# Optimization experiments

Hardware: AMD Instinct MI355X
Metric: run time of the kernel (lower is better)

Reference implementation:

```python
import jax, jax.numpy as jnp
import numpy as np

N = 100000
E = 3200000
CH_IN = 128
HID = 128
CH_OUT = 3


def setup_inputs() -> dict:
    key = jax.random.key(0)
    ks = jax.random.split(key, 16)
    def lin(kw, fan_in, fan_out):
        bound = 1.0 / np.sqrt(fan_in)
        kw1, kw2 = jax.random.split(kw)
        W = jax.random.uniform(kw1, (fan_in, fan_out), jnp.float32, -bound, bound)
        b = jax.random.uniform(kw2, (fan_out,), jnp.float32, -bound, bound)
        return W, b
    x = jax.random.normal(ks[0], (N, CH_IN), jnp.float32)
    edge_index = jax.random.randint(ks[1], (2, E), 0, N, jnp.int64)
    W1, b1 = lin(ks[2], CH_IN, HID)
    W2, b2 = lin(ks[3], HID, HID)
    lw1, lb1 = lin(ks[4], HID, HID)
    lw2, lb2 = lin(ks[5], HID, HID)
    lw3, lb3 = lin(ks[6], HID, HID)
    lw4, lb4 = lin(ks[7], HID, CH_OUT)
    return {"x": x, "edge_index": edge_index,
            "W1": W1, "b1": b1, "W2": W2, "b2": b2,
            "lw1": lw1, "lb1": lb1, "lw2": lw2, "lb2": lb2,
            "lw3": lw3, "lb3": lb3, "lw4": lw4, "lb4": lb4}


def gcn_conv(x, W, b, src, dst, n_nodes):
    xw = x @ W  # [N, H]
    ew = jnp.ones(src.shape[0], x.dtype)
    deg = jax.ops.segment_sum(ew, dst, num_segments=n_nodes) + 2.0  # +2 from improved self-loop
    dinv = jnp.where(deg > 0, jax.lax.rsqrt(deg), 0.0)
    norm = dinv[src] * dinv[dst]  # [E]
    agg = jax.ops.segment_sum(xw[src] * norm[:, None], dst, num_segments=n_nodes)
    # self-loop contribution: weight 2 * dinv[i]^2 * xw[i]
    agg = agg + xw * (2.0 * dinv * dinv)[:, None]
    return agg + b


def reference(x, edge_index, W1, b1, W2, b2, lw1, lb1, lw2, lb2, lw3, lb3, lw4, lb4):
    src, dst = edge_index[0], edge_index[1]
    n = x.shape[0]
    h = jnp.tanh(gcn_conv(x, W1, b1, src, dst, n))
    h = jnp.tanh(gcn_conv(h, W2, b2, src, dst, n))
    # dropout in eval mode = identity
    h = jnp.tanh(h @ lw1 + lb1)
    h = jnp.tanh(h @ lw2 + lb2)
    h = jnp.tanh(h @ lw3 + lb3)
    return h @ lw4 + lb4
```

## Files before the change

kernel.cpp:

```cpp
#include <hip/hip_runtime.h>

typedef __attribute__((ext_vector_type(8))) short short8;
typedef __attribute__((ext_vector_type(4))) float floatx4;
typedef __attribute__((ext_vector_type(4))) unsigned int uintx4;
typedef unsigned int uint32;

__device__ inline float b2f(unsigned short u) {
    union { uint32 i; float f; } x; x.i = ((uint32)u) << 16; return x.f;
}
__device__ inline float bl(uint32 v) {
    union { uint32 i; float f; } x; x.i = v << 16; return x.f;
}
__device__ inline float bh(uint32 v) {
    union { uint32 i; float f; } x; x.i = v & 0xffff0000u; return x.f;
}
__device__ inline unsigned short f2b(float f) {
    union { float f; uint32 u; } x; x.f = f;
    uint32 r = x.u + 0x7fffu + ((x.u >> 16) & 1u);
    return (unsigned short)(r >> 16);
}
__device__ inline float fast_tanh(float x) {
    float ax = __builtin_fabsf(x);
    float t = __builtin_amdgcn_exp2f(-2.8853900817779268f * ax);
    float r = (1.0f - t) * __builtin_amdgcn_rcpf(1.0f + t);
    return __builtin_copysignf(r, x);
}


#define CHUNK 8192
#define MAXBK 512
#define CAP   8704

__global__ __launch_bounds__(512, 2) void scatterb_k(const int* __restrict__ eidx,
                                                     uint32* __restrict__ bkt_cur,
                                                     uint32* __restrict__ packed, int E) {
    __shared__ uint32 hist[MAXBK];
    __shared__ uint32 hsc[MAXBK];
    __shared__ uint32 gbase[MAXBK];
    __shared__ uint32 lcur[MAXBK];
    __shared__ uint32 wsum[8];
    __shared__ uint32 stage[CHUNK];
    __shared__ unsigned short stgb[CHUNK];
    int t = threadIdx.x;
    int cbase = blockIdx.x * CHUNK;
    int n = E - cbase; if (n > CHUNK) n = CHUNK;

    hist[t] = 0;
    __syncthreads();
    int dreg[CHUNK / 512];
    int nt = 0;
    for (int i = t; i < n; i += 512) {
        int d = eidx[E + cbase + i];
        dreg[nt++] = d;
        atomicAdd(&hist[d >> 8], 1u);
    }
    __syncthreads();
    uint32 v = hist[t];
    uint32 x = v;
    int lane = t & 63;
#pragma unroll
    for (int off = 1; off < 64; off <<= 1) {
        uint32 y = __shfl_up(x, off);
        if (lane >= off) x += y;
    }
    if (lane == 63) wsum[t >> 6] = x;
    __syncthreads();
    uint32 pre = 0;
#pragma unroll
    for (int w = 0; w < 8; ++w) pre += (w < (t >> 6)) ? wsum[w] : 0;
    uint32 excl = x + pre - v;
    hsc[t] = excl;
    lcur[t] = excl;
    if (v) gbase[t] = (uint32)t * CAP + atomicAdd(&bkt_cur[t], v);
    __syncthreads();
    nt = 0;
    for (int i = t; i < n; i += 512) {
        int s = eidx[cbase + i];
        int d = dreg[nt++];
        int b = d >> 8;
        uint32 pos = atomicAdd(&lcur[b], 1u);
        stage[pos] = ((uint32)s << 8) | (uint32)(d & 255);
        stgb[pos] = (unsigned short)b;
    }
    __syncthreads();
    for (int i = t; i < n; i += 512) {
        int b = stgb[i];
        packed[gbase[b] + (i - hsc[b])] = stage[i];
    }
}


__global__ __launch_bounds__(256) void buildb_k(const uint32* __restrict__ packed,
                                                const uint32* __restrict__ bkt_cur,
                                                int* __restrict__ rowp,
                                                int* __restrict__ rowe,
                                                float* __restrict__ dinv,
                                                int* __restrict__ csr, int N,
                                                const float* __restrict__ w0,
                                                const float* __restrict__ w1,
                                                const float* __restrict__ w2,
                                                const float* __restrict__ w3,
                                                const float* __restrict__ w4,
                                                unsigned short* __restrict__ Wt_hi,
                                                unsigned short* __restrict__ Wt_lo) {
    __shared__ uint32 cnt[256];
    __shared__ uint32 cur[256];
    __shared__ uint32 wsum4[4];
    int t = threadIdx.x;
    int b = blockIdx.x;

    if (b < 40) {
        int widx = b >> 3;
        int f8 = ((b & 7) << 8) | t;
        const float* W;
        switch (widx) {
            case 0: W = w0; break;
            case 1: W = w1; break;
            case 2: W = w2; break;
            case 3: W = w3; break;
            default: W = w4; break;
        }
        int ct = f8 >> 8, kc = (f8 >> 6) & 3, quad = (f8 >> 4) & 3, r = f8 & 15;
        int c = ct * 16 + r;
        int kbase = kc * 32 + quad * 8;
        short8 hi8, lo8;
#pragma unroll
        for (int j = 0; j < 8; ++j) {
            float w = W[(kbase + j) * 128 + c];
            unsigned short h = f2b(w);
            hi8[j] = (short)h;
            lo8[j] = (short)f2b(w - b2f(h));
        }
        *(short8*)(Wt_hi + widx * 16384 + f8 * 8) = hi8;
        *(short8*)(Wt_lo + widx * 16384 + f8 * 8) = lo8;
    }

    uint32 base = (uint32)b * CAP;
    uint32 size = bkt_cur[b];
    int node0 = b << 8;

    cnt[t] = 0;
    __syncthreads();
    for (uint32 i = t; i < size; i += 256)
        atomicAdd(&cnt[packed[base + i] & 255u], 1u);
    __syncthreads();
    uint32 v = cnt[t];
    uint32 x = v;
    int lane = t & 63;
#pragma unroll
    for (int off = 1; off < 64; off <<= 1) {
        uint32 y = __shfl_up(x, off);
        if (lane >= off) x += y;
    }
    if (lane == 63) wsum4[t >> 6] = x;
    __syncthreads();
    uint32 pre = 0;
#pragma unroll
    for (int w = 0; w < 4; ++w) pre += (w < (t >> 6)) ? wsum4[w] : 0;
    uint32 loc = x + pre - v;
    cur[t] = loc;
    int node = node0 + t;
    if (node < N) {
        dinv[node] = rsqrtf((float)v + 2.0f);
        rowp[node] = (int)(base + loc);
        rowe[node] = (int)(base + loc + v);
    }
    __syncthreads();
    for (uint32 i = t; i < size; i += 256) {
        uint32 p = packed[base + i];
        uint32 pos = atomicAdd(&cur[p & 255u], 1u);
        csr[base + pos] = (int)(p >> 8);
    }
}


template <int ASRC>
__global__ __launch_bounds__(256, 4) void gemm_z_k(
    const void* __restrict__ Asrc,
    const unsigned short* __restrict__ Wt_hi,
    const unsigned short* __restrict__ Wt_lo,
    const float* __restrict__ dinv,
    unsigned short* __restrict__ out, int N) {
    int tid = threadIdx.x;
    if (blockIdx.x == 0 && tid < 64) {
        ((uint32*)out)[(size_t)N * 64 + tid] = 0;
    }
    int wave = tid >> 6, lane = tid & 63;
    int quad = lane >> 4, r = lane & 15;
    int m32 = blockIdx.x * 128 + wave * 32;

    short8 af[2][4];
#pragma unroll
    for (int s = 0; s < 2; ++s) {
        int rowA = m32 + s * 16 + r;
        if (rowA >= N) rowA = N - 1;
        if (ASRC == 0) {
            const float4* Af = (const float4*)Asrc;
#pragma unroll
            for (int kc = 0; kc < 4; ++kc) {
                float4 p0 = Af[((size_t)rowA * 128 + kc * 32 + quad * 8) >> 2];
                float4 p1 = Af[(((size_t)rowA * 128 + kc * 32 + quad * 8) >> 2) + 1];
                short8 a;
                a[0] = (short)f2b(p0.x); a[1] = (short)f2b(p0.y);
                a[2] = (short)f2b(p0.z); a[3] = (short)f2b(p0.w);
                a[4] = (short)f2b(p1.x); a[5] = (short)f2b(p1.y);
                a[6] = (short)f2b(p1.z); a[7] = (short)f2b(p1.w);
                af[s][kc] = a;
            }
        } else {
            const short* Ap = (const short*)Asrc;
#pragma unroll
            for (int kc = 0; kc < 4; ++kc)
                af[s][kc] = *(const short8*)(Ap + (size_t)rowA * 128 + kc * 32 + quad * 8);
        }
    }

    float dv[2][4];
#pragma unroll
    for (int s = 0; s < 2; ++s)
#pragma unroll
        for (int reg = 0; reg < 4; ++reg) {
            int i = m32 + s * 16 + quad * 4 + reg;
            dv[s][reg] = dinv[i < N ? i : N - 1];
        }

    const short8* WhF = (const short8*)Wt_hi + lane;
    const short8* WlF = (const short8*)Wt_lo + lane;

#pragma unroll
    for (int ct = 0; ct < 8; ++ct) {
        int n = ct * 16 + r;
        floatx4 a0 = {0.f, 0.f, 0.f, 0.f}, a1 = {0.f, 0.f, 0.f, 0.f};
#pragma unroll
        for (int kc = 0; kc < 4; ++kc) {
            short8 bh8 = WhF[(ct * 4 + kc) << 6];
            a0 = __builtin_amdgcn_mfma_f32_16x16x32_bf16(af[0][kc], bh8, a0, 0, 0, 0);
            a1 = __builtin_amdgcn_mfma_f32_16x16x32_bf16(af[1][kc], bh8, a1, 0, 0, 0);
            short8 bl8 = WlF[(ct * 4 + kc) << 6];
            a0 = __builtin_amdgcn_mfma_f32_16x16x32_bf16(af[0][kc], bl8, a0, 0, 0, 0);
            a1 = __builtin_amdgcn_mfma_f32_16x16x32_bf16(af[1][kc], bl8, a1, 0, 0, 0);
        }
#pragma unroll
        for (int reg = 0; reg < 4; ++reg) {
            int i0 = m32 + quad * 4 + reg;
            if (i0 < N) out[(size_t)i0 * 128 + n] = f2b(a0[reg] * dv[0][reg]);
            int i1 = m32 + 16 + quad * 4 + reg;
            if (i1 < N) out[(size_t)i1 * 128 + n] = f2b(a1[reg] * dv[1][reg]);
        }
    }
}


#define LSTR 136

__global__ __launch_bounds__(256, 2) void mlp_fused_k(
    const unsigned short* __restrict__ H,
    const unsigned short* __restrict__ WH,
    const unsigned short* __restrict__ WL,
    const float* __restrict__ lb1, const float* __restrict__ lb2,
    const float* __restrict__ lb3,
    const float* __restrict__ W4, const float* __restrict__ b4,
    float* __restrict__ out, int N) {
    __shared__ __align__(16) unsigned short wbuf[16384];
    __shared__ __align__(16) unsigned short tile[4][32 * LSTR];
    __shared__ float w4s[384];
    int tid = threadIdx.x;
    if (tid < 192) { w4s[tid] = W4[tid]; w4s[tid + 192] = W4[tid + 192]; }

    int wave = tid >> 6, lane = tid & 63;
    int quad = lane >> 4, r = lane & 15;
    unsigned short* T = tile[wave];
    int m32 = blockIdx.x * 128 + wave * 32;

    short8 af[2][4];
    const short* Hp = (const short*)H;
#pragma unroll
    for (int s = 0; s < 2; ++s) {
        int rowA = m32 + s * 16 + r;
        if (rowA >= N) rowA = N - 1;
#pragma unroll
        for (int kc = 0; kc < 4; ++kc)
            af[s][kc] = *(const short8*)(Hp + (size_t)rowA * 128 + kc * 32 + quad * 8);
    }

    const float* biases[3] = {lb1, lb2, lb3};
#pragma unroll
    for (int L = 0; L < 3; ++L) {
        const float* bias = biases[L];
        float bvv[8];
#pragma unroll
        for (int ct = 0; ct < 8; ++ct) bvv[ct] = bias[ct * 16 + r];
#pragma unroll
        for (int hf = 0; hf < 2; ++hf) {
            __syncthreads();
            {
                const uintx4* sh = (const uintx4*)(WH + L * 16384 + hf * 8192);
                const uintx4* sl = (const uintx4*)(WL + L * 16384 + hf * 8192);
                uintx4* dh = (uintx4*)wbuf;
                uintx4* dl = (uintx4*)(wbuf + 8192);
#pragma unroll
                for (int it = 0; it < 4; ++it) dh[tid + it * 256] = sh[tid + it * 256];
#pragma unroll
                for (int it = 0; it < 4; ++it) dl[tid + it * 256] = sl[tid + it * 256];
            }
            __syncthreads();
            const short8* whF = (const short8*)wbuf + lane;
            const short8* wlF = (const short8*)(wbuf + 8192) + lane;
#pragma unroll
            for (int c2 = 0; c2 < 4; ++c2) {
                int ct = hf * 4 + c2;
                int n = ct * 16 + r;
                floatx4 a0 = {0.f, 0.f, 0.f, 0.f}, a1 = {0.f, 0.f, 0.f, 0.f};
#pragma unroll
                for (int kc = 0; kc < 4; ++kc) {
                    short8 bh8 = whF[(c2 * 4 + kc) << 6];
                    a0 = __builtin_amdgcn_mfma_f32_16x16x32_bf16(af[0][kc], bh8, a0, 0, 0, 0);
                    a1 = __builtin_amdgcn_mfma_f32_16x16x32_bf16(af[1][kc], bh8, a1, 0, 0, 0);
                    short8 bl8 = wlF[(c2 * 4 + kc) << 6];
                    a0 = __builtin_amdgcn_mfma_f32_16x16x32_bf16(af[0][kc], bl8, a0, 0, 0, 0);
                    a1 = __builtin_amdgcn_mfma_f32_16x16x32_bf16(af[1][kc], bl8, a1, 0, 0, 0);
                }
                float bv = bvv[ct];
#pragma unroll
                for (int reg = 0; reg < 4; ++reg) {
                    int lrow = quad * 4 + reg;
                    T[lrow * LSTR + n] = f2b(fast_tanh(a0[reg] + bv));
                    T[(lrow + 16) * LSTR + n] = f2b(fast_tanh(a1[reg] + bv));
                }
            }
        }
        if (L < 2) {
#pragma unroll
            for (int s = 0; s < 2; ++s)
#pragma unroll
                for (int kc = 0; kc < 4; ++kc)
                    af[s][kc] = *(const short8*)&T[(s * 16 + r) * LSTR + kc * 32 + quad * 8];
        }
    }

    int lrow = lane & 31;
    int halfc = lane >> 5;
    float a0 = 0.f, a1 = 0.f, a2 = 0.f;
#pragma unroll
    for (int c8 = 0; c8 < 8; ++c8) {
        int cbase = halfc * 64 + c8 * 8;
        short8 hv = *(const short8*)&T[lrow * LSTR + cbase];
#pragma unroll
        for (int j = 0; j < 8; ++j) {
            float xv = b2f((unsigned short)hv[j]);
            int ch = cbase + j;
            a0 = fmaf(xv, w4s[ch * 3 + 0], a0);
            a1 = fmaf(xv, w4s[ch * 3 + 1], a1);
            a2 = fmaf(xv, w4s[ch * 3 + 2], a2);
        }
    }
    a0 += __shfl_xor(a0, 32);
    a1 += __shfl_xor(a1, 32);
    a2 += __shfl_xor(a2, 32);
    if (halfc == 0) {
        int i = m32 + lrow;
        if (i < N) {
            out[(size_t)i * 3 + 0] = a0 + b4[0];
            out[(size_t)i * 3 + 1] = a1 + b4[1];
            out[(size_t)i * 3 + 2] = a2 + b4[2];
        }
    }
}


template <int NT>
__global__ __launch_bounds__(256) void agg_full_k(
    const uint32* __restrict__ z, const int* __restrict__ rowp,
    const int* __restrict__ rowe, const int* __restrict__ csr,
    const float* __restrict__ dinv, const float* __restrict__ bias,
    uint32* __restrict__ out, int N) {
    int lane = threadIdx.x & 63;
    int i = blockIdx.x * 4 + (threadIdx.x >> 6);
    if (i >= N) return;
    int start = rowp[i], end = rowe[i];
    const uint32* zl = z + lane;
    float a0 = 0.f, a1 = 0.f;
    for (int e = start; e < end; e += 64) {
        int cnt = end - e;
        if (cnt > 64) cnt = 64;
        int s;
        if (lane < cnt) {
            s = NT ? __builtin_nontemporal_load(&csr[e + lane]) : csr[e + lane];
        } else {
            s = N;
        }
        int mp = (cnt + 15) & ~15;
        for (int m = 0; m < mp; m += 16) {
            uint32 v[16];
#pragma unroll
            for (int p = 0; p < 16; ++p) {
                int sj = __shfl(s, m + p);
                v[p] = zl[(size_t)sj << 6];
            }
#pragma unroll
            for (int p = 0; p < 16; ++p) {
                a0 += bl(v[p]);
                a1 += bh(v[p]);
            }
        }
    }
    uint32 vi = zl[(size_t)i << 6];
    a0 += 2.f * bl(vi);
    a1 += 2.f * bh(vi);
    float di = dinv[i];
    float2 bv = ((const float2*)bias)[lane];
    float h0 = fast_tanh(fmaf(di, a0, bv.x));
    float h1 = fast_tanh(fmaf(di, a1, bv.y));
    uint32 pv = (uint32)f2b(h0) | ((uint32)f2b(h1) << 16);
    if (NT) {
        __builtin_nontemporal_store(pv, &out[((size_t)i << 6) + lane]);
    } else {
        out[((size_t)i << 6) + lane] = pv;
    }
}

extern "C" void kernel_launch(void* const* d_in, const int* in_sizes, int n_in,
                              void* d_out, int out_size, void* d_ws, size_t ws_size,
                              hipStream_t stream) {
    const float* x   = (const float*)d_in[0];
    const int* eidx  = (const int*)d_in[1];
    const float* W1  = (const float*)d_in[2];
    const float* b1  = (const float*)d_in[3];
    const float* W2  = (const float*)d_in[4];
    const float* b2  = (const float*)d_in[5];
    const float* lw1 = (const float*)d_in[6];
    const float* lb1 = (const float*)d_in[7];
    const float* lw2 = (const float*)d_in[8];
    const float* lb2 = (const float*)d_in[9];
    const float* lw3 = (const float*)d_in[10];
    const float* lb3 = (const float*)d_in[11];
    const float* lw4 = (const float*)d_in[12];
    const float* lb4 = (const float*)d_in[13];
    float* out = (float*)d_out;

    const int N = in_sizes[0] / 128;
    const int E = in_sizes[1] / 2;

    char* p = (char*)d_ws;
    auto alloc = [&](size_t bytes) -> void* {
        void* q = (void*)p;
        p += (bytes + 255) & ~(size_t)255;
        return q;
    };
    const int NBK = (N + 255) >> 8;
    float* dinv      = (float*)alloc((size_t)N * 4);
    int* rowp        = (int*)alloc((size_t)N * 4);
    int* rowe        = (int*)alloc((size_t)N * 4);
    uint32* bkt_cur  = (uint32*)alloc(MAXBK * 4);
    int* csr         = (int*)alloc((size_t)NBK * CAP * 4);
    unsigned short* Wt_hi = (unsigned short*)alloc(5 * 16384 * 2);
    unsigned short* Wt_lo = (unsigned short*)alloc(5 * 16384 * 2);
    unsigned short* bufA  = (unsigned short*)alloc((size_t)(N + 1) * 128 * 2);
    unsigned short* bufB  = (unsigned short*)alloc((size_t)(N + 1) * 128 * 2);
    uint32* packed = (uint32*)bufA;

    const int MB4 = (N + 127) / 128;
    const int AB  = (N + 3) / 4;
    const int NCH = (E + CHUNK - 1) / CHUNK;

    hipMemsetAsync(bkt_cur, 0, MAXBK * 4, stream);
    scatterb_k<<<NCH, 512, 0, stream>>>(eidx, bkt_cur, packed, E);
    buildb_k<<<NBK, 256, 0, stream>>>(packed, bkt_cur, rowp, rowe, dinv, csr, N,
                                      W1, W2, lw1, lw2, lw3, Wt_hi, Wt_lo);

    const unsigned short* WH = Wt_hi;
    const unsigned short* WL = Wt_lo;

    gemm_z_k<0><<<MB4, 256, 0, stream>>>(x, WH + 0 * 16384, WL + 0 * 16384, dinv, bufA, N);
    agg_full_k<1><<<AB, 256, 0, stream>>>((const uint32*)bufA, rowp, rowe, csr, dinv, b1,
                                          (uint32*)bufB, N);
    gemm_z_k<1><<<MB4, 256, 0, stream>>>(bufB, WH + 1 * 16384, WL + 1 * 16384, dinv, bufA, N);
    agg_full_k<0><<<AB, 256, 0, stream>>>((const uint32*)bufA, rowp, rowe, csr, dinv, b2,
                                          (uint32*)bufB, N);
    mlp_fused_k<<<MB4, 256, 0, stream>>>(bufB, WH + 2 * 16384, WL + 2 * 16384,
                                         lb1, lb2, lb3, lw4, lb4, out, N);
}
```

Measured before the change: 454.8 us.

## Fuse GCN aggregation into following GEMM and MLP kernels via shared-memory tiles

The first aggregation is fused with the second layer's feature transform, and the second aggregation is fused into the MLP kernel. Aggregated rows are written to a shared-memory tile instead of a global buffer, which removes two kernel launches and a full N×128 bf16 write and read round-trip per fusion. In exchange each block serialises the gathers for its rows inside one or a few waves, with fewer rows in flight per wave. The MLP kernel's occupancy is limited by its large shared memory, so gather latency hiding may drop. The second aggregation also widens its unroll to 32 loads and drops the nontemporal hints.

Result: slower. 506.5 us (+11.4%).

```diff
diff --git a/kernel.cpp b/kernel.cpp
--- a/kernel.cpp
+++ b/kernel.cpp
@@ -30,6 +30,7 @@
 #define CHUNK 8192
 #define MAXBK 512
 #define CAP   8704
+#define LSTR  136
 
 __global__ __launch_bounds__(512, 2) void scatterb_k(const int* __restrict__ eidx,
                                                      uint32* __restrict__ bkt_cur,
@@ -251,10 +252,97 @@
 }
 
 
-#define LSTR 136
-
-__global__ __launch_bounds__(256, 2) void mlp_fused_k(
-    const unsigned short* __restrict__ H,
+__global__ __launch_bounds__(256, 4) void agg_gemm_k(
+    const uint32* __restrict__ z, const int* __restrict__ rowp,
+    const int* __restrict__ rowe, const int* __restrict__ csr,
+    const float* __restrict__ dinv, const float* __restrict__ bias,
+    const unsigned short* __restrict__ Wt_hi,
+    const unsigned short* __restrict__ Wt_lo,
+    unsigned short* __restrict__ out, int N) {
+    __shared__ __align__(16) unsigned short tile[32 * LSTR];
+    int tid = threadIdx.x;
+    if (blockIdx.x == 0 && tid < 64) ((uint32*)out)[(size_t)N * 64 + tid] = 0;
+    int wave = tid >> 6, lane = tid & 63;
+    int base = blockIdx.x * 32;
+    const uint32* zl = z + lane;
+    float2 bv = ((const float2*)bias)[lane];
+#pragma unroll 1
+    for (int k = 0; k < 8; ++k) {
+        int i = base + wave * 8 + k;
+        if (i >= N) break;
+        int start = rowp[i], end = rowe[i];
+        float a0 = 0.f, a1 = 0.f;
+        for (int e = start; e < end; e += 64) {
+            int cnt = end - e; if (cnt > 64) cnt = 64;
+            int s = (lane < cnt) ? csr[e + lane] : N;
+            int mp = (cnt + 15) & ~15;
+            for (int m = 0; m < mp; m += 16) {
+                uint32 v[16];
+#pragma unroll
+                for (int p = 0; p < 16; ++p) {
+                    int sj = __shfl(s, m + p);
+                    v[p] = zl[(size_t)sj << 6];
+                }
+#pragma unroll
+                for (int p = 0; p < 16; ++p) { a0 += bl(v[p]); a1 += bh(v[p]); }
+            }
+        }
+        uint32 vi = zl[(size_t)i << 6];
+        a0 += 2.f * bl(vi);
+        a1 += 2.f * bh(vi);
+        float di = dinv[i];
+        float h0 = fast_tanh(fmaf(di, a0, bv.x));
+        float h1 = fast_tanh(fmaf(di, a1, bv.y));
+        ((uint32*)(tile + (wave * 8 + k) * LSTR))[lane] =
+            (uint32)f2b(h0) | ((uint32)f2b(h1) << 16);
+    }
+    __syncthreads();
+    int quad = lane >> 4, r = lane & 15;
+    short8 af[2][4];
+#pragma unroll
+    for (int s = 0; s < 2; ++s)
+#pragma unroll
+        for (int kc = 0; kc < 4; ++kc)
+            af[s][kc] = *(const short8*)&tile[(s * 16 + r) * LSTR + kc * 32 + quad * 8];
+    float dv[2][4];
+#pragma unroll
+    for (int s = 0; s < 2; ++s)
+#pragma unroll
+        for (int reg = 0; reg < 4; ++reg) {
+            int i = base + s * 16 + quad * 4 + reg;
+            dv[s][reg] = dinv[i < N ? i : N - 1];
+        }
+    const short8* WhF = (const short8*)Wt_hi + lane;
+    const short8* WlF = (const short8*)Wt_lo + lane;
+#pragma unroll
+    for (int c2 = 0; c2 < 2; ++c2) {
+        int ct = wave * 2 + c2;
+        int n = ct * 16 + r;
+        floatx4 a0 = {0.f, 0.f, 0.f, 0.f}, a1 = {0.f, 0.f, 0.f, 0.f};
+#pragma unroll
+        for (int kc = 0; kc < 4; ++kc) {
+            short8 bh8 = WhF[(ct * 4 + kc) << 6];
+            a0 = __builtin_amdgcn_mfma_f32_16x16x32_bf16(af[0][kc], bh8, a0, 0, 0, 0);
+            a1 = __builtin_amdgcn_mfma_f32_16x16x32_bf16(af[1][kc], bh8, a1, 0, 0, 0);
+            short8 bl8 = WlF[(ct * 4 + kc) << 6];
+            a0 = __builtin_amdgcn_mfma_f32_16x16x32_bf16(af[0][kc], bl8, a0, 0, 0, 0);
+            a1 = __builtin_amdgcn_mfma_f32_16x16x32_bf16(af[1][kc], bl8, a1, 0, 0, 0);
+        }
+#pragma unroll
+        for (int reg = 0; reg < 4; ++reg) {
+            int i0 = base + quad * 4 + reg;
+            if (i0 < N) out[(size_t)i0 * 128 + n] = f2b(a0[reg] * dv[0][reg]);
+            int i1 = base + 16 + quad * 4 + reg;
+            if (i1 < N) out[(size_t)i1 * 128 + n] = f2b(a1[reg] * dv[1][reg]);
+        }
+    }
+}
+
+
+__global__ __launch_bounds__(256, 2) void agg_mlp_k(
+    const uint32* __restrict__ z, const int* __restrict__ rowp,
+    const int* __restrict__ rowe, const int* __restrict__ csr,
+    const float* __restrict__ dinv, const float* __restrict__ bias0,
     const unsigned short* __restrict__ WH,
     const unsigned short* __restrict__ WL,
     const float* __restrict__ lb1, const float* __restrict__ lb2,
@@ -272,16 +360,46 @@
     unsigned short* T = tile[wave];
     int m32 = blockIdx.x * 128 + wave * 32;
 
+    {
+        const uint32* zl = z + lane;
+        float2 bv = ((const float2*)bias0)[lane];
+#pragma unroll 1
+        for (int k = 0; k < 32; ++k) {
+            int i = m32 + k;
+            if (i >= N) break;
+            int start = rowp[i], end = rowe[i];
+            float a0 = 0.f, a1 = 0.f;
+            for (int e = start; e < end; e += 64) {
+                int cnt = end - e; if (cnt > 64) cnt = 64;
+                int s = (lane < cnt) ? csr[e + lane] : N;
+                int mp = (cnt + 31) & ~31;
+                for (int m = 0; m < mp; m += 32) {
+                    uint32 v[32];
+#pragma unroll
+                    for (int p = 0; p < 32; ++p) {
+                        int sj = __shfl(s, m + p);
+                        v[p] = zl[(size_t)sj << 6];
+                    }
+#pragma unroll
+                    for (int p = 0; p < 32; ++p) { a0 += bl(v[p]); a1 += bh(v[p]); }
+                }
+            }
+            uint32 vi = zl[(size_t)i << 6];
+            a0 += 2.f * bl(vi);
+            a1 += 2.f * bh(vi);
+            float di = dinv[i];
+            float h0 = fast_tanh(fmaf(di, a0, bv.x));
+            float h1 = fast_tanh(fmaf(di, a1, bv.y));
+            ((uint32*)(T + k * LSTR))[lane] = (uint32)f2b(h0) | ((uint32)f2b(h1) << 16);
+        }
+    }
+
     short8 af[2][4];
-    const short* Hp = (const short*)H;
-#pragma unroll
-    for (int s = 0; s < 2; ++s) {
-        int rowA = m32 + s * 16 + r;
-        if (rowA >= N) rowA = N - 1;
+#pragma unroll
+    for (int s = 0; s < 2; ++s)
 #pragma unroll
         for (int kc = 0; kc < 4; ++kc)
-            af[s][kc] = *(const short8*)(Hp + (size_t)rowA * 128 + kc * 32 + quad * 8);
-    }
+            af[s][kc] = *(const short8*)&T[(s * 16 + r) * LSTR + kc * 32 + quad * 8];
 
     const float* biases[3] = {lb1, lb2, lb3};
 #pragma unroll
@@ -364,58 +482,6 @@
             out[(size_t)i * 3 + 1] = a1 + b4[1];
             out[(size_t)i * 3 + 2] = a2 + b4[2];
         }
-    }
-}
-
-
-template <int NT>
-__global__ __launch_bounds__(256) void agg_full_k(
-    const uint32* __restrict__ z, const int* __restrict__ rowp,
-    const int* __restrict__ rowe, const int* __restrict__ csr,
-    const float* __restrict__ dinv, const float* __restrict__ bias,
-    uint32* __restrict__ out, int N) {
-    int lane = threadIdx.x & 63;
-    int i = blockIdx.x * 4 + (threadIdx.x >> 6);
-    if (i >= N) return;
-    int start = rowp[i], end = rowe[i];
-    const uint32* zl = z + lane;
-    float a0 = 0.f, a1 = 0.f;
-    for (int e = start; e < end; e += 64) {
-        int cnt = end - e;
-        if (cnt > 64) cnt = 64;
-        int s;
-        if (lane < cnt) {
-            s = NT ? __builtin_nontemporal_load(&csr[e + lane]) : csr[e + lane];
-        } else {
-            s = N;
-        }
-        int mp = (cnt + 15) & ~15;
-        for (int m = 0; m < mp; m += 16) {
-            uint32 v[16];
-#pragma unroll
-            for (int p = 0; p < 16; ++p) {
-                int sj = __shfl(s, m + p);
-                v[p] = zl[(size_t)sj << 6];
-            }
-#pragma unroll
-            for (int p = 0; p < 16; ++p) {
-                a0 += bl(v[p]);
-                a1 += bh(v[p]);
-            }
-        }
-    }
-    uint32 vi = zl[(size_t)i << 6];
-    a0 += 2.f * bl(vi);
-    a1 += 2.f * bh(vi);
-    float di = dinv[i];
-    float2 bv = ((const float2*)bias)[lane];
-    float h0 = fast_tanh(fmaf(di, a0, bv.x));
-    float h1 = fast_tanh(fmaf(di, a1, bv.y));
-    uint32 pv = (uint32)f2b(h0) | ((uint32)f2b(h1) << 16);
-    if (NT) {
-        __builtin_nontemporal_store(pv, &out[((size_t)i << 6) + lane]);
-    } else {
-        out[((size_t)i << 6) + lane] = pv;
     }
 }
 
@@ -459,9 +525,9 @@
     unsigned short* bufB  = (unsigned short*)alloc((size_t)(N + 1) * 128 * 2);
     uint32* packed = (uint32*)bufA;
 
-    const int MB4 = (N + 127) / 128;
-    const int AB  = (N + 3) / 4;
-    const int NCH = (E + CHUNK - 1) / CHUNK;
+    const int MB4  = (N + 127) / 128;
+    const int NB32 = (N + 31) / 32;
+    const int NCH  = (E + CHUNK - 1) / CHUNK;
 
     hipMemsetAsync(bkt_cur, 0, MAXBK * 4, stream);
     scatterb_k<<<NCH, 512, 0, stream>>>(eidx, bkt_cur, packed, E);
@@ -472,11 +538,9 @@
     const unsigned short* WL = Wt_lo;
 
     gemm_z_k<0><<<MB4, 256, 0, stream>>>(x, WH + 0 * 16384, WL + 0 * 16384, dinv, bufA, N);
-    agg_full_k<1><<<AB, 256, 0, stream>>>((const uint32*)bufA, rowp, rowe, csr, dinv, b1,
-                                          (uint32*)bufB, N);
-    gemm_z_k<1><<<MB4, 256, 0, stream>>>(bufB, WH + 1 * 16384, WL + 1 * 16384, dinv, bufA, N);
-    agg_full_k<0><<<AB, 256, 0, stream>>>((const uint32*)bufA, rowp, rowe, csr, dinv, b2,
-                                          (uint32*)bufB, N);
-    mlp_fused_k<<<MB4, 256, 0, stream>>>(bufB, WH + 2 * 16384, WL + 2 * 16384,
-                                         lb1, lb2, lb3, lw4, lb4, out, N);
-}
+    agg_gemm_k<<<NB32, 256, 0, stream>>>((const uint32*)bufA, rowp, rowe, csr, dinv, b1,
+                                         WH + 1 * 16384, WL + 1 * 16384, bufB, N);
+    agg_mlp_k<<<MB4, 256, 0, stream>>>((const uint32*)bufB, rowp, rowe, csr, dinv, b2,
+                                       WH + 2 * 16384, WL + 2 * 16384,
+                                       lb1, lb2, lb3, lw4, lb4, out, N);
+}
```

## Overlap first GEMM with CSR build by moving dinv scaling into aggregation

Applied to the files above, without the earlier changes.

Weight bf16 hi/lo splitting moves into the scatter kernel. The first GEMM runs as extra blocks of the CSR-build kernel, so the x·W1 product overlaps bucket sorting and one launch goes away. To allow this, the GEMM no longer pre-scales rows by dinv; the aggregation instead loads dinv for each source neighbour and uses an FMA, with a zero-padded dinv[N] for the padding lanes. This adds a gathered dinv load per edge in both aggregation passes and drops the nontemporal load/store hints.

Result: no change. 453.0 us (-0.4%).

```diff
diff --git a/kernel.cpp b/kernel.cpp
--- a/kernel.cpp
+++ b/kernel.cpp
@@ -30,10 +30,18 @@
 #define CHUNK 8192
 #define MAXBK 512
 #define CAP   8704
+#define LSTR  136
 
 __global__ __launch_bounds__(512, 2) void scatterb_k(const int* __restrict__ eidx,
                                                      uint32* __restrict__ bkt_cur,
-                                                     uint32* __restrict__ packed, int E) {
+                                                     uint32* __restrict__ packed, int E,
+                                                     const float* __restrict__ w0,
+                                                     const float* __restrict__ w1,
+                                                     const float* __restrict__ w2,
+                                                     const float* __restrict__ w3,
+                                                     const float* __restrict__ w4,
+                                                     unsigned short* __restrict__ Wt_hi,
+                                                     unsigned short* __restrict__ Wt_lo) {
     __shared__ uint32 hist[MAXBK];
     __shared__ uint32 hsc[MAXBK];
     __shared__ uint32 gbase[MAXBK];
@@ -42,6 +50,34 @@
     __shared__ uint32 stage[CHUNK];
     __shared__ unsigned short stgb[CHUNK];
     int t = threadIdx.x;
+
+    if (blockIdx.x < 20) {
+        int u = blockIdx.x * 512 + t;
+        int widx = u >> 11;
+        int f8 = u & 2047;
+        const float* W;
+        switch (widx) {
+            case 0: W = w0; break;
+            case 1: W = w1; break;
+            case 2: W = w2; break;
+            case 3: W = w3; break;
+            default: W = w4; break;
+        }
+        int ct = f8 >> 8, kc = (f8 >> 6) & 3, quad = (f8 >> 4) & 3, r = f8 & 15;
+        int c = ct * 16 + r;
+        int kbase = kc * 32 + quad * 8;
+        short8 hi8, lo8;
+#pragma unroll
+        for (int j = 0; j < 8; ++j) {
+            float w = W[(kbase + j) * 128 + c];
+            unsigned short h = f2b(w);
+            hi8[j] = (short)h;
+            lo8[j] = (short)f2b(w - b2f(h));
+        }
+        *(short8*)(Wt_hi + widx * 16384 + f8 * 8) = hi8;
+        *(short8*)(Wt_lo + widx * 16384 + f8 * 8) = lo8;
+    }
+
     int cbase = blockIdx.x * CHUNK;
     int n = E - cbase; if (n > CHUNK) n = CHUNK;
 
@@ -90,112 +126,33 @@
 }
 
 
-__global__ __launch_bounds__(256) void buildb_k(const uint32* __restrict__ packed,
-                                                const uint32* __restrict__ bkt_cur,
-                                                int* __restrict__ rowp,
-                                                int* __restrict__ rowe,
-                                                float* __restrict__ dinv,
-                                                int* __restrict__ csr, int N,
-                                                const float* __restrict__ w0,
-                                                const float* __restrict__ w1,
-                                                const float* __restrict__ w2,
-                                                const float* __restrict__ w3,
-                                                const float* __restrict__ w4,
-                                                unsigned short* __restrict__ Wt_hi,
-                                                unsigned short* __restrict__ Wt_lo) {
+__global__ __launch_bounds__(256) void buildb_gemm_k(
+    const uint32* __restrict__ packed,
+    const uint32* __restrict__ bkt_cur,
+    int* __restrict__ rowp, int* __restrict__ rowe,
+    float* __restrict__ dinv, int* __restrict__ csr, int N, int NBK,
+    const float* __restrict__ x,
+    const unsigned short* __restrict__ Wt_hi,
+    const unsigned short* __restrict__ Wt_lo,
+    unsigned short* __restrict__ z1out) {
     __shared__ uint32 cnt[256];
     __shared__ uint32 cur[256];
     __shared__ uint32 wsum4[4];
     int t = threadIdx.x;
     int b = blockIdx.x;
 
-    if (b < 40) {
-        int widx = b >> 3;
-        int f8 = ((b & 7) << 8) | t;
-        const float* W;
-        switch (widx) {
-            case 0: W = w0; break;
-            case 1: W = w1; break;
-            case 2: W = w2; break;
-            case 3: W = w3; break;
-            default: W = w4; break;
-        }
-        int ct = f8 >> 8, kc = (f8 >> 6) & 3, quad = (f8 >> 4) & 3, r = f8 & 15;
-        int c = ct * 16 + r;
-        int kbase = kc * 32 + quad * 8;
-        short8 hi8, lo8;
-#pragma unroll
-        for (int j = 0; j < 8; ++j) {
-            float w = W[(kbase + j) * 128 + c];
-            unsigned short h = f2b(w);
-            hi8[j] = (short)h;
-            lo8[j] = (short)f2b(w - b2f(h));
-        }
-        *(short8*)(Wt_hi + widx * 16384 + f8 * 8) = hi8;
-        *(short8*)(Wt_lo + widx * 16384 + f8 * 8) = lo8;
-    }
-
-    uint32 base = (uint32)b * CAP;
-    uint32 size = bkt_cur[b];
-    int node0 = b << 8;
-
-    cnt[t] = 0;
-    __syncthreads();
-    for (uint32 i = t; i < size; i += 256)
-        atomicAdd(&cnt[packed[base + i] & 255u], 1u);
-    __syncthreads();
-    uint32 v = cnt[t];
-    uint32 x = v;
-    int lane = t & 63;
-#pragma unroll
-    for (int off = 1; off < 64; off <<= 1) {
-        uint32 y = __shfl_up(x, off);
-        if (lane >= off) x += y;
-    }
-    if (lane == 63) wsum4[t >> 6] = x;
-    __syncthreads();
-    uint32 pre = 0;
-#pragma unroll
-    for (int w = 0; w < 4; ++w) pre += (w < (t >> 6)) ? wsum4[w] : 0;
-    uint32 loc = x + pre - v;
-    cur[t] = loc;
-    int node = node0 + t;
-    if (node < N) {
-        dinv[node] = rsqrtf((float)v + 2.0f);
-        rowp[node] = (int)(base + loc);
-        rowe[node] = (int)(base + loc + v);
-    }
-    __syncthreads();
-    for (uint32 i = t; i < size; i += 256) {
-        uint32 p = packed[base + i];
-        uint32 pos = atomicAdd(&cur[p & 255u], 1u);
-        csr[base + pos] = (int)(p >> 8);
-    }
-}
-
-
-template <int ASRC>
-__global__ __launch_bounds__(256, 4) void gemm_z_k(
-    const void* __restrict__ Asrc,
-    const unsigned short* __restrict__ Wt_hi,
-    const unsigned short* __restrict__ Wt_lo,
-    const float* __restrict__ dinv,
-    unsigned short* __restrict__ out, int N) {
-    int tid = threadIdx.x;
-    if (blockIdx.x == 0 && tid < 64) {
-        ((uint32*)out)[(size_t)N * 64 + tid] = 0;
-    }
-    int wave = tid >> 6, lane = tid & 63;
-    int quad = lane >> 4, r = lane & 15;
-    int m32 = blockIdx.x * 128 + wave * 32;
-
-    short8 af[2][4];
-#pragma unroll
-    for (int s = 0; s < 2; ++s) {
-        int rowA = m32 + s * 16 + r;
-        if (rowA >= N) rowA = N - 1;
-        if (ASRC == 0) {
-            const float4* Af = (const float4*)Asrc;
+    if (b >= NBK) {
+        int gb = b - NBK;
+        if (gb == 0 && t < 64) ((uint32*)z1out)[(size_t)N * 64 + t] = 0;
+        int wave = t >> 6, lane = t & 63;
+        int quad = lane >> 4, r = lane & 15;
+        int m32 = gb * 128 + wave * 32;
+        short8 af[2][4];
+        const float4* Af = (const float4*)x;
+#pragma unroll
+        for (int s = 0; s < 2; ++s) {
+            int rowA = m32 + s * 16 + r;
+            if (rowA >= N) rowA = N - 1;
 #pragma unroll
             for (int kc = 0; kc < 4; ++kc) {
                 float4 p0 = Af[((size_t)rowA * 128 + kc * 32 + quad * 8) >> 2];
@@ -207,22 +164,96 @@
                 a[6] = (short)f2b(p1.z); a[7] = (short)f2b(p1.w);
                 af[s][kc] = a;
             }
-        } else {
-            const short* Ap = (const short*)Asrc;
-#pragma unroll
-            for (int kc = 0; kc < 4; ++kc)
-                af[s][kc] = *(const short8*)(Ap + (size_t)rowA * 128 + kc * 32 + quad * 8);
-        }
-    }
-
-    float dv[2][4];
-#pragma unroll
-    for (int s = 0; s < 2; ++s)
-#pragma unroll
-        for (int reg = 0; reg < 4; ++reg) {
-            int i = m32 + s * 16 + quad * 4 + reg;
-            dv[s][reg] = dinv[i < N ? i : N - 1];
-        }
+        }
+        const short8* WhF = (const short8*)Wt_hi + lane;
+        const short8* WlF = (const short8*)Wt_lo + lane;
+#pragma unroll
+        for (int ct = 0; ct < 8; ++ct) {
+            int n = ct * 16 + r;
+            floatx4 a0 = {0.f, 0.f, 0.f, 0.f}, a1 = {0.f, 0.f, 0.f, 0.f};
+#pragma unroll
+            for (int kc = 0; kc < 4; ++kc) {
+                short8 bh8 = WhF[(ct * 4 + kc) << 6];
+                a0 = __builtin_amdgcn_mfma_f32_16x16x32_bf16(af[0][kc], bh8, a0, 0, 0, 0);
+                a1 = __builtin_amdgcn_mfma_f32_16x16x32_bf16(af[1][kc], bh8, a1, 0, 0, 0);
+                short8 bl8 = WlF[(ct * 4 + kc) << 6];
+                a0 = __builtin_amdgcn_mfma_f32_16x16x32_bf16(af[0][kc], bl8, a0, 0, 0, 0);
+                a1 = __builtin_amdgcn_mfma_f32_16x16x32_bf16(af[1][kc], bl8, a1, 0, 0, 0);
+            }
+#pragma unroll
+            for (int reg = 0; reg < 4; ++reg) {
+                int i0 = m32 + quad * 4 + reg;
+                if (i0 < N) z1out[(size_t)i0 * 128 + n] = f2b(a0[reg]);
+                int i1 = m32 + 16 + quad * 4 + reg;
+                if (i1 < N) z1out[(size_t)i1 * 128 + n] = f2b(a1[reg]);
+            }
+        }
+        return;
+    }
+
+    if (b == 0 && t == 0) dinv[N] = 0.f;
+    uint32 base = (uint32)b * CAP;
+    uint32 size = bkt_cur[b];
+    int node0 = b << 8;
+
+    cnt[t] = 0;
+    __syncthreads();
+    for (uint32 i = t; i < size; i += 256)
+        atomicAdd(&cnt[packed[base + i] & 255u], 1u);
+    __syncthreads();
+    uint32 v = cnt[t];
+    uint32 x2 = v;
+    int lane = t & 63;
+#pragma unroll
+    for (int off = 1; off < 64; off <<= 1) {
+        uint32 y = __shfl_up(x2, off);
+        if (lane >= off) x2 += y;
+    }
+    if (lane == 63) wsum4[t >> 6] = x2;
+    __syncthreads();
+    uint32 pre = 0;
+#pragma unroll
+    for (int w = 0; w < 4; ++w) pre += (w < (t >> 6)) ? wsum4[w] : 0;
+    uint32 loc = x2 + pre - v;
+    cur[t] = loc;
+    int node = node0 + t;
+    if (node < N) {
+        dinv[node] = rsqrtf((float)v + 2.0f);
+        rowp[node] = (int)(base + loc);
+        rowe[node] = (int)(base + loc + v);
+    }
+    __syncthreads();
+    for (uint32 i = t; i < size; i += 256) {
+        uint32 p = packed[base + i];
+        uint32 pos = atomicAdd(&cur[p & 255u], 1u);
+        csr[base + pos] = (int)(p >> 8);
+    }
+}
+
+
+__global__ __launch_bounds__(256, 4) void gemm_z_k(
+    const unsigned short* __restrict__ Asrc,
+    const unsigned short* __restrict__ Wt_hi,
+    const unsigned short* __restrict__ Wt_lo,
+    unsigned short* __restrict__ out, int N) {
+    int tid = threadIdx.x;
+    if (blockIdx.x == 0 && tid < 64) {
+        ((uint32*)out)[(size_t)N * 64 + tid] = 0;
+    }
+    int wave = tid >> 6, lane = tid & 63;
+    int quad = lane >> 4, r = lane & 15;
+    int m32 = blockIdx.x * 128 + wave * 32;
+
+    short8 af[2][4];
+    const short* Ap = (const short*)Asrc;
+#pragma unroll
+    for (int s = 0; s < 2; ++s) {
+        int rowA = m32 + s * 16 + r;
+        if (rowA >= N) rowA = N - 1;
+#pragma unroll
+        for (int kc = 0; kc < 4; ++kc)
+            af[s][kc] = *(const short8*)(Ap + (size_t)rowA * 128 + kc * 32 + quad * 8);
+    }
 
     const short8* WhF = (const short8*)Wt_hi + lane;
     const short8* WlF = (const short8*)Wt_lo + lane;
@@ -243,15 +274,13 @@
 #pragma unroll
         for (int reg = 0; reg < 4; ++reg) {
             int i0 = m32 + quad * 4 + reg;
-            if (i0 < N) out[(size_t)i0 * 128 + n] = f2b(a0[reg] * dv[0][reg]);
+            if (i0 < N) out[(size_t)i0 * 128 + n] = f2b(a0[reg]);
             int i1 = m32 + 16 + quad * 4 + reg;
-            if (i1 < N) out[(size_t)i1 * 128 + n] = f2b(a1[reg] * dv[1][reg]);
-        }
-    }
-}
-
-
-#define LSTR 136
+            if (i1 < N) out[(size_t)i1 * 128 + n] = f2b(a1[reg]);
+        }
+    }
+}
+
 
 __global__ __launch_bounds__(256, 2) void mlp_fused_k(
     const unsigned short* __restrict__ H,
@@ -368,7 +397,6 @@
 }
 
 
-template <int NT>
 __global__ __launch_bounds__(256) void agg_full_k(
     const uint32* __restrict__ z, const int* __restrict__ rowp,
     const int* __restrict__ rowe, const int* __restrict__ csr,
@@ -383,40 +411,34 @@
     for (int e = start; e < end; e += 64) {
         int cnt = end - e;
         if (cnt > 64) cnt = 64;
-        int s;
-        if (lane < cnt) {
-            s = NT ? __builtin_nontemporal_load(&csr[e + lane]) : csr[e + lane];
-        } else {
-            s = N;
-        }
+        int s = (lane < cnt) ? csr[e + lane] : N;
+        float dv = dinv[s];
         int mp = (cnt + 15) & ~15;
         for (int m = 0; m < mp; m += 16) {
             uint32 v[16];
+            float dvp[16];
 #pragma unroll
             for (int p = 0; p < 16; ++p) {
                 int sj = __shfl(s, m + p);
+                dvp[p] = __shfl(dv, m + p);
                 v[p] = zl[(size_t)sj << 6];
             }
 #pragma unroll
             for (int p = 0; p < 16; ++p) {
-                a0 += bl(v[p]);
-                a1 += bh(v[p]);
-            }
-        }
-    }
+                a0 = fmaf(dvp[p], bl(v[p]), a0);
+                a1 = fmaf(dvp[p], bh(v[p]), a1);
+            }
+        }
+    }
+    float di = dinv[i];
     uint32 vi = zl[(size_t)i << 6];
-    a0 += 2.f * bl(vi);
-    a1 += 2.f * bh(vi);
-    float di = dinv[i];
+    float di2 = 2.f * di;
+    a0 = fmaf(di2, bl(vi), a0);
+    a1 = fmaf(di2, bh(vi), a1);
     float2 bv = ((const float2*)bias)[lane];
     float h0 = fast_tanh(fmaf(di, a0, bv.x));
     float h1 = fast_tanh(fmaf(di, a1, bv.y));
-    uint32 pv = (uint32)f2b(h0) | ((uint32)f2b(h1) << 16);
-    if (NT) {
-        __builtin_nontemporal_store(pv, &out[((size_t)i << 6) + lane]);
-    } else {
-        out[((size_t)i << 6) + lane] = pv;
-    }
+    out[((size_t)i << 6) + lane] = (uint32)f2b(h0) | ((uint32)f2b(h1) << 16);
 }
 
 extern "C" void kernel_launch(void* const* d_in, const int* in_sizes, int n_in,
@@ -448,7 +470,7 @@
         return q;
     };
     const int NBK = (N + 255) >> 8;
-    float* dinv      = (float*)alloc((size_t)N * 4);
+    float* dinv      = (float*)alloc((size_t)(N + 1) * 4);
     int* rowp        = (int*)alloc((size_t)N * 4);
     int* rowe        = (int*)alloc((size_t)N * 4);
     uint32* bkt_cur  = (uint32*)alloc(MAXBK * 4);
@@ -457,26 +479,28 @@
     unsigned short* Wt_lo = (unsigned short*)alloc(5 * 16384 * 2);
     unsigned short* bufA  = (unsigned short*)alloc((size_t)(N + 1) * 128 * 2);
     unsigned short* bufB  = (unsigned short*)alloc((size_t)(N + 1) * 128 * 2);
-    uint32* packed = (uint32*)bufA;
+    uint32* packed = (uint32*)bufB;
 
     const int MB4 = (N + 127) / 128;
     const int AB  = (N + 3) / 4;
     const int NCH = (E + CHUNK - 1) / CHUNK;
 
     hipMemsetAsync(bkt_cur, 0, MAXBK * 4, stream);
-    scatterb_k<<<NCH, 512, 0, stream>>>(eidx, bkt_cur, packed, E);
-    buildb_k<<<NBK, 256, 0, stream>>>(packed, bkt_cur, rowp, rowe, dinv, csr, N,
-                                      W1, W2, lw1, lw2, lw3, Wt_hi, Wt_lo);
+    scatterb_k<<<NCH, 512, 0, stream>>>(eidx, bkt_cur, packed, E,
+                                        W1, W2, lw1, lw2, lw3, Wt_hi, Wt_lo);
+    buildb_gemm_k<<<NBK + MB4, 256, 0, stream>>>(packed, bkt_cur, rowp, rowe, dinv,
+                                                 csr, N, NBK, x,
+                                                 Wt_hi + 0 * 16384, Wt_lo + 0 * 16384,
+                                                 bufA);
 
     const unsigned short* WH = Wt_hi;
     const unsigned short* WL = Wt_lo;
 
-    gemm_z_k<0><<<MB4, 256, 0, stream>>>(x, WH + 0 * 16384, WL + 0 * 16384, dinv, bufA, N);
-    agg_full_k<1><<<AB, 256, 0, stream>>>((const uint32*)bufA, rowp, rowe, csr, dinv, b1,
-                                          (uint32*)bufB, N);
-    gemm_z_k<1><<<MB4, 256, 0, stream>>>(bufB, WH + 1 * 16384, WL + 1 * 16384, dinv, bufA, N);
-    agg_full_k<0><<<AB, 256, 0, stream>>>((const uint32*)bufA, rowp, rowe, csr, dinv, b2,
-                                          (uint32*)bufB, N);
+    agg_full_k<<<AB, 256, 0, stream>>>((const uint32*)bufA, rowp, rowe, csr, dinv, b1,
+                                       (uint32*)bufB, N);
+    gemm_z_k<<<MB4, 256, 0, stream>>>(bufB, WH + 1 * 16384, WL + 1 * 16384, bufA, N);
+    agg_full_k<<<AB, 256, 0, stream>>>((const uint32*)bufA, rowp, rowe, csr, dinv, b2,
+                                       (uint32*)bufB, N);
     mlp_fused_k<<<MB4, 256, 0, stream>>>(bufB, WH + 2 * 16384, WL + 2 * 16384,
                                          lb1, lb2, lb3, lw4, lb4, out, N);
 }
```
